# Optimization experiments

Measured on AMD Instinct MI355X. Metric: run time of the kernel, lower is better.

The kernel has to match this reference:

```python
import jax, jax.numpy as jnp
import numpy as np

B, T, D, H, L = 4, 2048, 256, 4, 2
HD = D // H
VOCAB, MAX_BITS, MLP_H = 32, 64, 64


def setup_inputs() -> dict:
    key = jax.random.key(0)
    ks = jax.random.split(key, 20)
    s = 0.02
    n = lambda k, shp: (jax.random.normal(k, shp, jnp.float32) * s)
    inp = {
        'tokens': jax.random.randint(ks[0], (B, T), 0, VOCAB),
        'embed': n(ks[1], (VOCAB, D)),
        'ln1_w': jnp.ones((L, D)), 'ln1_b': jnp.zeros((L, D)),
        'qkv_w': n(ks[2], (L, D, 3 * D)), 'qkv_b': jnp.zeros((L, 3 * D)),
        'proj_w': n(ks[3], (L, D, D)), 'proj_b': jnp.zeros((L, D)),
        'ln2_w': jnp.ones((L, D)), 'ln2_b': jnp.zeros((L, D)),
        'ffn1_w': n(ks[4], (L, D, 4 * D)), 'ffn1_b': jnp.zeros((L, 4 * D)),
        'ffn2_w': n(ks[5], (L, 4 * D, D)), 'ffn2_b': jnp.zeros((L, D)),
        'lnf_w': jnp.ones((D,)), 'lnf_b': jnp.zeros((D,)),
        'out_queries': n(ks[6], (MAX_BITS * 2, D)),
        'outp_w': n(ks[7], (D, 1)), 'outp_b': jnp.zeros((1,)),
        'mlp_w1': n(ks[8], (3, MLP_H)), 'mlp_b1': jnp.zeros((MLP_H,)),
        'mlp_w2': n(ks[9], (MLP_H, MLP_H)), 'mlp_b2': jnp.zeros((MLP_H,)),
        'mlp_w3': n(ks[10], (MLP_H, 2)), 'mlp_b3': jnp.zeros((2,)),
    }
    return inp


def _layernorm(x, w, b, eps=1e-5):
    mu = jnp.mean(x, axis=-1, keepdims=True)
    var = jnp.mean(jnp.square(x - mu), axis=-1, keepdims=True)
    return (x - mu) * jax.lax.rsqrt(var + eps) * w + b


def _rope_tables(t_len, hd):
    inv_freq = 1.0 / (10000.0 ** (jnp.arange(0, hd, 2, dtype=jnp.float32) / hd))
    freqs = jnp.outer(jnp.arange(t_len, dtype=jnp.float32), inv_freq)  # [T, hd/2]
    emb = jnp.concatenate([freqs, freqs], axis=-1)                     # [T, hd]
    return jnp.cos(emb)[None, :, None, :], jnp.sin(emb)[None, :, None, :]


def _rotate_half(x):
    x1, x2 = x[..., : x.shape[-1] // 2], x[..., x.shape[-1] // 2:]
    return jnp.concatenate([-x2, x1], axis=-1)


def _attention(x, qkv_w, qkv_b, proj_w, proj_b):
    b, t, c = x.shape
    qkv = (x @ qkv_w + qkv_b).reshape(b, t, 3, H, HD)
    q, k, v = qkv[:, :, 0], qkv[:, :, 1], qkv[:, :, 2]  # [B,T,H,HD]
    cos, sin = _rope_tables(t, HD)
    q = q * cos + _rotate_half(q) * sin
    k = k * cos + _rotate_half(k) * sin
    scores = jnp.einsum('bthd,bshd->bhts', q, k) / jnp.sqrt(jnp.float32(HD))
    causal = jnp.tril(jnp.ones((t, t), dtype=bool))
    scores = jnp.where(causal, scores, -jnp.inf)
    attn = jax.nn.softmax(scores, axis=-1)
    out = jnp.einsum('bhts,bshd->bthd', attn, v).reshape(b, t, c)
    return out @ proj_w + proj_b


def reference(tokens, embed, ln1_w, ln1_b, qkv_w, qkv_b, proj_w, proj_b,
              ln2_w, ln2_b, ffn1_w, ffn1_b, ffn2_w, ffn2_b, lnf_w, lnf_b,
              out_queries, outp_w, outp_b,
              mlp_w1, mlp_b1, mlp_w2, mlp_b2, mlp_w3, mlp_b3):
    x = embed[tokens]  # [B,T,D]
    for l in range(L):
        x = x + _attention(_layernorm(x, ln1_w[l], ln1_b[l]),
                           qkv_w[l], qkv_b[l], proj_w[l], proj_b[l])
        h = _layernorm(x, ln2_w[l], ln2_b[l])
        h = jax.nn.gelu(h @ ffn1_w[l] + ffn1_b[l], approximate=False)
        x = x + (h @ ffn2_w[l] + ffn2_b[l])
    x = _layernorm(x, lnf_w, lnf_b)
    # query cross-attention for bit-pair selection
    q_scores = jnp.einsum('qd,btd->bqt', out_queries, x) / jnp.sqrt(jnp.float32(D))
    q_attn = jax.nn.softmax(q_scores, axis=-1)           # [B, 2*MAX_BITS, T]
    selected = jnp.einsum('bqt,btd->bqd', q_attn, x)
    bits = jax.nn.sigmoid((selected @ outp_w + outp_b)[..., 0])
    pairs = bits.reshape(-1, MAX_BITS, 2)                # [B, MAX_BITS, 2]

    # sequential full-adder over bits
    def step(carry, ab):  # carry [B], ab [B,2]
        z = jnp.concatenate([ab, carry[:, None]], axis=-1)  # [B,3]
        h = jax.nn.relu(z @ mlp_w1 + mlp_b1)
        h = jax.nn.relu(h @ mlp_w2 + mlp_b2)
        o = jax.nn.sigmoid(h @ mlp_w3 + mlp_b3)
        return o[:, 1], o[:, 0]

    carry0 = jnp.zeros((pairs.shape[0],), jnp.float32)
    carry, sum_bits = jax.lax.scan(step, carry0, jnp.swapaxes(pairs, 0, 1))
    sum_all = jnp.concatenate([sum_bits.T, carry[:, None]], axis=1)  # [B, MAX_BITS+1]
    return sum_all, pairs, q_attn
```

## Files before the change

### kernel.cpp

```cpp
#include <hip/hip_runtime.h>
#include <hip/hip_bf16.h>

#define BB 4
#define TT 2048
#define DD 256
#define HH 4
#define HDD 64
#define NROW 8192
#define NQ 128

typedef __hip_bfloat16 bf16;
typedef __attribute__((ext_vector_type(8))) short bf8v;
typedef __attribute__((ext_vector_type(4))) short bf4v;
typedef __attribute__((ext_vector_type(4))) float f4v;
typedef __attribute__((ext_vector_type(2))) unsigned int u2v;

__device__ __forceinline__ bf16 f2b(float v){ return __float2bfloat16(v); }
__device__ __forceinline__ short f2bs(float v){
    bf16 h = __float2bfloat16(v);
    return *reinterpret_cast<short*>(&h);
}
__device__ __forceinline__ float bs2f(short s){
    bf16 h = *reinterpret_cast<bf16*>(&s);
    return __bfloat162float(h);
}
__device__ __forceinline__ float rl(float v, int l){
    return __uint_as_float(__builtin_amdgcn_readlane(__float_as_uint(v), l));
}

#define DPP_ROR_ADD(v, ctrl) \
    ((v) + __int_as_float(__builtin_amdgcn_update_dpp(0, __float_as_int(v), (ctrl), 0xF, 0xF, false)))
#define DPP_ROR_MAX(v, ctrl) \
    fmaxf((v), __int_as_float(__builtin_amdgcn_update_dpp(0, __float_as_int(v), (ctrl), 0xF, 0xF, false)))

__device__ __forceinline__ void plswap16(float v, float& a, float& b){
#if __has_builtin(__builtin_amdgcn_permlane16_swap)
    u2v r = __builtin_amdgcn_permlane16_swap(__float_as_uint(v), __float_as_uint(v), false, false);
    a = __uint_as_float(r.x); b = __uint_as_float(r.y);
#else
    a = v; b = v;
    asm volatile("" : "+v"(b));
    asm("v_permlane16_swap_b32 %0, %1" : "+v"(a), "+v"(b));
#endif
}
__device__ __forceinline__ void plswap32(float v, float& a, float& b){
#if __has_builtin(__builtin_amdgcn_permlane32_swap)
    u2v r = __builtin_amdgcn_permlane32_swap(__float_as_uint(v), __float_as_uint(v), false, false);
    a = __uint_as_float(r.x); b = __uint_as_float(r.y);
#else
    a = v; b = v;
    asm volatile("" : "+v"(b));
    asm("v_permlane32_swap_b32 %0, %1" : "+v"(a), "+v"(b));
#endif
}
__device__ __forceinline__ float swap16_add(float v){ float a,b; plswap16(v,a,b); return a + b; }
__device__ __forceinline__ float swap32_add(float v){ float a,b; plswap32(v,a,b); return a + b; }
__device__ __forceinline__ float swap16_max(float v){ float a,b; plswap16(v,a,b); return fmaxf(a,b); }
__device__ __forceinline__ float swap32_max(float v){ float a,b; plswap32(v,a,b); return fmaxf(a,b); }
__device__ __forceinline__ float wsum(float v){
    v = DPP_ROR_ADD(v, 0x121); v = DPP_ROR_ADD(v, 0x122);
    v = DPP_ROR_ADD(v, 0x124); v = DPP_ROR_ADD(v, 0x128);
    v = swap16_add(v); v = swap32_add(v);
    return v;
}
__device__ __forceinline__ float wmax(float v){
    v = DPP_ROR_MAX(v, 0x121); v = DPP_ROR_MAX(v, 0x122);
    v = DPP_ROR_MAX(v, 0x124); v = DPP_ROR_MAX(v, 0x128);
    v = swap16_max(v); v = swap32_max(v);
    return v;
}

#define MFMA32(A,B,C) __builtin_amdgcn_mfma_f32_16x16x32_bf16((A),(B),(C),0,0,0)
#if __has_builtin(__builtin_amdgcn_mfma_f32_16x16x16bf16_1k)
#define MFMA16(A,B,C) __builtin_amdgcn_mfma_f32_16x16x16bf16_1k((A),(B),(C),0,0,0)
#else
__device__ __forceinline__ f4v mfma16_asm(bf4v a, bf4v b, f4v c){
    f4v d;
    asm("v_mfma_f32_16x16x16_bf16 %0, %1, %2, %3" : "=v"(d) : "v"(a), "v"(b), "v"(c));
    return d;
}
#define MFMA16(A,B,C) mfma16_asm((A),(B),(C))
#endif

__global__ __launch_bounds__(256) void k_embln(const int* __restrict__ tok,
                                               const float* __restrict__ emb,
                                               const float* __restrict__ w,
                                               const float* __restrict__ b,
                                               float* __restrict__ x,
                                               bf16* __restrict__ Y){
    int row = blockIdx.x*4 + (threadIdx.x >> 6);
    int lane = threadIdx.x & 63;
    f4v v = *(const f4v*)(emb + (long)tok[row]*DD + lane*4);
    *(f4v*)(x + (long)row*DD + lane*4) = v;
    float s  = (v[0]+v[1]) + (v[2]+v[3]);
    float s2 = (v[0]*v[0]+v[1]*v[1]) + (v[2]*v[2]+v[3]*v[3]);
    s = wsum(s); s2 = wsum(s2);
    float mu  = s * (1.0f/DD);
    float var = s2 * (1.0f/DD) - mu*mu;
    float rs  = rsqrtf(var + 1e-5f);
    f4v wv4 = *(const f4v*)(w + lane*4);
    f4v bv4 = *(const f4v*)(b + lane*4);
    bf4v o;
    #pragma unroll
    for (int i=0;i<4;i++) o[i] = f2bs((v[i]-mu)*rs*wv4[i] + bv4[i]);
    *(bf4v*)(Y + (long)row*DD + lane*4) = o;
}

__global__ __launch_bounds__(256) void k_wtall(const float* __restrict__ qkvw,
                                               const float* __restrict__ projw,
                                               const float* __restrict__ f1w,
                                               const float* __restrict__ f2w,
                                               bf16* __restrict__ wt,
                                               const float* __restrict__ oq, bf16* __restrict__ oqb,
                                               float* __restrict__ cosT, float* __restrict__ sinT,
                                               const float* __restrict__ w2, float* __restrict__ w2t){
    __shared__ float t[32][33];
    int z = blockIdx.z;
    if (z == 8){
        int bid = blockIdx.y*32 + blockIdx.x;
        if (bid >= 256) return;
        int gid = bid*256 + threadIdx.y*32 + threadIdx.x;
        int tt = gid >> 5, dd = gid & 31;
        float invf = powf(10000.0f, -(float)(2*dd)/64.0f);
        float ang = (float)tt * invf;
        float sn, cs;
        sincosf(ang, &sn, &cs);
        cosT[gid] = cs; sinT[gid] = sn;
        if (gid < NQ*DD) oqb[gid] = f2b(oq[gid]);
        if (gid < 4096){ int j = gid >> 6, k = gid & 63; w2t[gid] = w2[k*64 + j]; }
        return;
    }
    int l = z >> 2, type = z & 3;
    long L = (long)l*786432;
    int K, M; const float* src; long doff;
    if (type == 0){ K=256;  M=768;  src = qkvw + (long)l*256*768;  doff = L; }
    else if (type == 1){ K=256;  M=256;  src = projw + (long)l*256*256; doff = L + 196608; }
    else if (type == 2){ K=256;  M=1024; src = f1w  + (long)l*256*1024; doff = L + 262144; }
    else               { K=1024; M=256;  src = f2w  + (long)l*1024*256; doff = L + 524288; }
    int m0 = blockIdx.x*32, k0 = blockIdx.y*32;
    if (m0 >= M || k0 >= K) return;
    bf16* dst = wt + doff;
    int tx = threadIdx.x, ty = threadIdx.y;
    #pragma unroll
    for (int i=0;i<4;i++)
        t[ty+i*8][tx] = src[(long)(k0+ty+i*8)*M + m0 + tx];
    __syncthreads();
    #pragma unroll
    for (int i=0;i<4;i++)
        dst[(long)(m0+ty+i*8)*K + k0 + tx] = f2b(t[tx][ty+i*8]);
}

__global__ __launch_bounds__(256) void k_lnb(const float* __restrict__ X,
                                             const float* __restrict__ w,
                                             const float* __restrict__ b,
                                             bf16* __restrict__ Y){
    int row = blockIdx.x*4 + (threadIdx.x >> 6);
    int lane = threadIdx.x & 63;
    f4v v = *(const f4v*)(X + (long)row*DD + lane*4);
    float s  = (v[0]+v[1]) + (v[2]+v[3]);
    float s2 = (v[0]*v[0]+v[1]*v[1]) + (v[2]*v[2]+v[3]*v[3]);
    s = wsum(s); s2 = wsum(s2);
    float mu  = s * (1.0f/DD);
    float var = s2 * (1.0f/DD) - mu*mu;
    float rs  = rsqrtf(var + 1e-5f);
    f4v wv4 = *(const f4v*)(w + lane*4);
    f4v bv4 = *(const f4v*)(b + lane*4);
    bf4v o;
    #pragma unroll
    for (int i=0;i<4;i++) o[i] = f2bs((v[i]-mu)*rs*wv4[i] + bv4[i]);
    *(bf4v*)(Y + (long)row*DD + lane*4) = o;
}

__global__ __launch_bounds__(256) void k_lnf(const float* __restrict__ X,
                                             const float* __restrict__ w,
                                             const float* __restrict__ b,
                                             const float* __restrict__ ow,
                                             bf16* __restrict__ Yb,
                                             float* __restrict__ g){
    int row = blockIdx.x*4 + (threadIdx.x >> 6);
    int lane = threadIdx.x & 63;
    f4v v = *(const f4v*)(X + (long)row*DD + lane*4);
    float s  = (v[0]+v[1]) + (v[2]+v[3]);
    float s2 = (v[0]*v[0]+v[1]*v[1]) + (v[2]*v[2]+v[3]*v[3]);
    s = wsum(s); s2 = wsum(s2);
    float mu  = s * (1.0f/DD);
    float var = s2 * (1.0f/DD) - mu*mu;
    float rs  = rsqrtf(var + 1e-5f);
    f4v wv4 = *(const f4v*)(w + lane*4);
    f4v bv4 = *(const f4v*)(b + lane*4);
    f4v ov4 = *(const f4v*)(ow + lane*4);
    bf4v o;
    float gp = 0.f;
    #pragma unroll
    for (int i=0;i<4;i++){
        float y = (v[i]-mu)*rs*wv4[i] + bv4[i];
        o[i] = f2bs(y);
        gp += y * ov4[i];
    }
    *(bf4v*)(Yb + (long)row*DD + lane*4) = o;
    gp = wsum(gp);
    if (lane == 0) g[row] = gp;
}

__global__ __launch_bounds__(256) void k_mgemm(const bf16* __restrict__ A,
                                               const bf16* __restrict__ Wt,
                                               const float* __restrict__ bias,
                                               float* __restrict__ Cf,
                                               bf16* __restrict__ Cb,
                                               int K, int M, int mode){
    __shared__ short As[2][128*64];
    __shared__ short Ws[2][64*64];
    int tid = threadIdx.x;
    int lane = tid & 63, wv = tid >> 6;
    int n0 = blockIdx.y * 128, m0 = blockIdx.x * 64;
    int rbase = (wv >> 1) * 64, cbase = (wv & 1) * 32;
    f4v acc[4][2] = {};
    bf8v va[4], vw[2];
    #pragma unroll
    for (int c=0;c<4;c++){
        int idx = c*256 + tid;
        va[c] = *(const bf8v*)(A + (long)(n0 + (idx>>3))*K + ((idx&7)<<3));
    }
    #pragma unroll
    for (int c=0;c<2;c++){
        int idx = c*256 + tid;
        vw[c] = *(const bf8v*)(Wt + (long)(m0 + (idx>>3))*K + ((idx&7)<<3));
    }
    int buf = 0;
    for (int k0 = 0; k0 < K; k0 += 64){
        #pragma unroll
        for (int c=0;c<4;c++){
            int idx = c*256 + tid, row = idx>>3;
            *(bf8v*)&As[buf][row*64 + (((idx&7)<<3) ^ ((row&7)<<3))] = va[c];
        }
        #pragma unroll
        for (int c=0;c<2;c++){
            int idx = c*256 + tid, row = idx>>3;
            *(bf8v*)&Ws[buf][row*64 + (((idx&7)<<3) ^ ((row&7)<<3))] = vw[c];
        }
        __syncthreads();
        if (k0 + 64 < K){
            #pragma unroll
            for (int c=0;c<4;c++){
                int idx = c*256 + tid;
                va[c] = *(const bf8v*)(A + (long)(n0 + (idx>>3))*K + k0 + 64 + ((idx&7)<<3));
            }
            #pragma unroll
            for (int c=0;c<2;c++){
                int idx = c*256 + tid;
                vw[c] = *(const bf8v*)(Wt + (long)(m0 + (idx>>3))*K + k0 + 64 + ((idx&7)<<3));
            }
        }
        int k8 = (lane >> 4) << 3;
        #pragma unroll
        for (int h=0; h<2; h++){
            bf8v af[4], bfr[2];
            #pragma unroll
            for (int i=0;i<4;i++){
                int row = rbase + i*16 + (lane&15);
                af[i] = *(bf8v*)&As[buf][row*64 + ((h*32 + k8) ^ ((row&7)<<3))];
            }
            #pragma unroll
            for (int j=0;j<2;j++){
                int row = cbase + j*16 + (lane&15);
                bfr[j] = *(bf8v*)&Ws[buf][row*64 + ((h*32 + k8) ^ ((row&7)<<3))];
            }
            #pragma unroll
            for (int i=0;i<4;i++)
                #pragma unroll
                for (int j=0;j<2;j++)
                    acc[i][j] = MFMA32(af[i], bfr[j], acc[i][j]);
        }
        buf ^= 1;
    }
    int rq = (lane >> 4) * 4;
    int cl = lane & 15;
    #pragma unroll
    for (int i=0;i<4;i++){
        #pragma unroll
        for (int j=0;j<2;j++){
            int m = m0 + cbase + j*16 + cl;
            float bs = bias[m];
            #pragma unroll
            for (int r=0;r<4;r++){
                int n = n0 + rbase + i*16 + rq + r;
                float v = acc[i][j][r] + bs;
                long idx = (long)n*M + m;
                if (mode == 0)      Cf[idx] = v;
                else if (mode == 1) Cf[idx] += v;
                else if (mode == 2) Cb[idx] = f2b(0.5f*v*(1.0f + erff(v*0.70710678118654752f)));
                else                Cb[idx] = f2b(v);
            }
        }
    }
}

__global__ __launch_bounds__(256) void k_mgemmQKV(const bf16* __restrict__ A,
                                                  const bf16* __restrict__ Wt,
                                                  const float* __restrict__ bias,
                                                  const float* __restrict__ cosT,
                                                  const float* __restrict__ sinT,
                                                  bf16* __restrict__ qb,
                                                  bf16* __restrict__ kb,
                                                  bf16* __restrict__ vt){
    __shared__ short As[128*64];
    __shared__ short Ws[64*64];
    __shared__ short E[128][68];
    const int K = 256, M = 768;
    int tid = threadIdx.x;
    int lane = tid & 63, wv = tid >> 6;
    int n0 = blockIdx.y * 128, m0 = blockIdx.x * 64;
    int rbase = (wv >> 1) * 64, cbase = (wv & 1) * 32;
    f4v acc[4][2] = {};
    for (int k0 = 0; k0 < K; k0 += 64){
        bf8v va[4], vw[2];
        #pragma unroll
        for (int c=0;c<4;c++){
            int idx = c*256 + tid;
            va[c] = *(const bf8v*)(A + (long)(n0 + (idx>>3))*K + k0 + ((idx&7)<<3));
        }
        #pragma unroll
        for (int c=0;c<2;c++){
            int idx = c*256 + tid;
            vw[c] = *(const bf8v*)(Wt + (long)(m0 + (idx>>3))*K + k0 + ((idx&7)<<3));
        }
        __syncthreads();
        #pragma unroll
        for (int c=0;c<4;c++){
            int idx = c*256 + tid, row = idx>>3;
            *(bf8v*)&As[row*64 + (((idx&7)<<3) ^ ((row&7)<<3))] = va[c];
        }
        #pragma unroll
        for (int c=0;c<2;c++){
            int idx = c*256 + tid, row = idx>>3;
            *(bf8v*)&Ws[row*64 + (((idx&7)<<3) ^ ((row&7)<<3))] = vw[c];
        }
        __syncthreads();
        int k8 = (lane >> 4) << 3;
        #pragma unroll
        for (int h=0; h<2; h++){
            bf8v af[4], bfr[2];
            #pragma unroll
            for (int i=0;i<4;i++){
                int row = rbase + i*16 + (lane&15);
                af[i] = *(bf8v*)&As[row*64 + ((h*32 + k8) ^ ((row&7)<<3))];
            }
            #pragma unroll
            for (int j=0;j<2;j++){
                int row = cbase + j*16 + (lane&15);
                bfr[j] = *(bf8v*)&Ws[row*64 + ((h*32 + k8) ^ ((row&7)<<3))];
            }
            #pragma unroll
            for (int i=0;i<4;i++)
                #pragma unroll
                for (int j=0;j<2;j++)
                    acc[i][j] = MFMA32(af[i], bfr[j], acc[i][j]);
        }
    }
    int rq = (lane >> 4) * 4;
    int cl = lane & 15;
    #pragma unroll
    for (int i=0;i<4;i++){
        #pragma unroll
        for (int j=0;j<2;j++){
            int cc = cbase + j*16 + cl;
            float bs = bias[m0 + cc];
            #pragma unroll
            for (int r=0;r<4;r++)
                E[rbase + i*16 + rq + r][cc] = f2bs(acc[i][j][r] + bs);
        }
    }
    __syncthreads();
    int part = m0 >> 8;
    int h = (m0 >> 6) & 3;
    int b = n0 >> 11;
    int t0 = n0 & 2047;
    int bh = b*HH + h;
    if (part < 2){
        bf16* dst0 = part ? kb : qb;
        int r2 = tid >> 2;
        int c0 = (tid & 3) * 16;
        int cpx = c0 ^ 32;
        #pragma unroll
        for (int half=0; half<2; half++){
            int row = half*64 + r2;
            int t = t0 + row;
            bf8v e0 = *(bf8v*)&E[row][c0];
            bf8v e1 = *(bf8v*)&E[row][c0+8];
            bf8v p0 = *(bf8v*)&E[row][cpx];
            bf8v p1 = *(bf8v*)&E[row][cpx+8];
            const float* ct = cosT + t*32;
            const float* st = sinT + t*32;
            short o[16];
            #pragma unroll
            for (int i=0;i<8;i++){
                int d = c0 + i, dd = d & 31;
                float cs = ct[dd], sn = st[dd];
                float v = bs2f(e0[i]), v2 = bs2f(p0[i]);
                o[i] = f2bs((d < 32) ? (v*cs - v2*sn) : (v*cs + v2*sn));
            }
            #pragma unroll
            for (int i=0;i<8;i++){
                int d = c0 + 8 + i, dd = d & 31;
                float cs = ct[dd], sn = st[dd];
                float v = bs2f(e1[i]), v2 = bs2f(p1[i]);
                o[8+i] = f2bs((d < 32) ? (v*cs - v2*sn) : (v*cs + v2*sn));
            }
            short* dp = (short*)dst0 + ((long)bh*TT + t)*64 + c0;
            *(bf8v*)dp     = *(bf8v*)&o[0];
            *(bf8v*)(dp+8) = *(bf8v*)&o[8];
        }
    } else {
        int tIdx0 = t0 >> 6;
        int d  = (tid & 127) >> 1;
        int k0 = (tid & 1) * 32;
        int tt = tid >> 7;
        short o[32];
        #pragma unroll
        for (int k=0;k<32;k++) o[k] = E[tt*64 + k0 + k][d];
        short* dp = (short*)vt + (((long)bh*32 + tIdx0 + tt)*64 + d)*64 + k0;
        *(bf8v*)dp      = *(bf8v*)&o[0];
        *(bf8v*)(dp+8)  = *(bf8v*)&o[8];
        *(bf8v*)(dp+16) = *(bf8v*)&o[16];
        *(bf8v*)(dp+24) = *(bf8v*)&o[24];
    }
}

__global__ __launch_bounds__(256) void k_fattn(const bf16* __restrict__ qb,
                                               const bf16* __restrict__ kb,
                                               const bf16* __restrict__ vt,
                                               bf16* __restrict__ ob){
    __shared__ short Ks[2][64][72];
    __shared__ short Vs[2][64][68];
    int bh = blockIdx.y;
    int qt = (int)(gridDim.x - 1) - (int)blockIdx.x;
    int tid = threadIdx.x;
    int lane = tid & 63, w = tid >> 6;
    int col = lane & 15, quad = lane >> 4;
    int q0 = qt*64 + w*16;
    const bf16* qp = qb + ((long)bh*TT + q0 + col)*64 + quad*8;
    bf8v bq0 = *(const bf8v*)(qp);
    bf8v bq1 = *(const bf8v*)(qp + 32);
    f4v oc[4] = {};
    float lsum = 0.f;
    int qglob = q0 + col;
    int srow = tid >> 2, sc0 = (tid & 3) * 16;
    const short* kgb = (const short*)kb + ((long)bh*TT + srow)*64 + sc0;
    const short* vgb = (const short*)vt + (((long)bh*32)*64 + srow)*64 + sc0;

    bf8v pk0 = *(const bf8v*)kgb;
    bf8v pk1 = *(const bf8v*)(kgb + 8);
    bf8v pv0 = *(const bf8v*)vgb;
    bf8v pv1 = *(const bf8v*)(vgb + 8);
    *(bf8v*)&Ks[0][srow][sc0]     = pk0;
    *(bf8v*)&Ks[0][srow][sc0 + 8] = pk1;
    *(bf8v*)&Vs[0][srow][sc0]     = pv0;
    *(bf8v*)&Vs[0][srow][sc0 + 8] = pv1;

    int buf = 0;
    for (int kt=0; kt<=qt; kt++){
        __syncthreads();
        bool more = (kt < qt);
        if (more){
            const short* kg = kgb + (long)(kt+1)*4096;
            const short* vg = vgb + (long)(kt+1)*4096;
            pk0 = *(const bf8v*)kg;
            pk1 = *(const bf8v*)(kg + 8);
            pv0 = *(const bf8v*)vg;
            pv1 = *(const bf8v*)(vg + 8);
        }
        bool diag = (kt == qt);
        int ntmax = diag ? w : 3;
        bf4v bp[4];
        #pragma unroll
        for (int nt=0; nt<4; nt++){
            if (nt > ntmax) continue;
            bf8v ka0 = *(const bf8v*)&Ks[buf][nt*16 + col][quad*8];
            bf8v ka1 = *(const bf8v*)&Ks[buf][nt*16 + col][32 + quad*8];
            f4v st = {};
            st = MFMA32(ka0, bq0, st);
            st = MFMA32(ka1, bq1, st);
            int key0 = kt*64 + nt*16 + quad*4;
            bf4v pb;
            #pragma unroll
            for (int r=0; r<4; r++){
                float e = __expf(st[r]*0.125f);
                if (diag && (key0 + r > qglob)) e = 0.f;
                lsum += e;
                pb[r] = f2bs(e);
            }
            bp[nt] = pb;
        }
        #pragma unroll
        for (int dt=0; dt<4; dt++){
            #pragma unroll
            for (int nt=0; nt<4; nt++){
                if (nt > ntmax) continue;
                bf4v va = *(const bf4v*)&Vs[buf][dt*16 + col][nt*16 + quad*4];
                oc[dt] = MFMA16(va, bp[nt], oc[dt]);
            }
        }
        if (more){
            *(bf8v*)&Ks[buf^1][srow][sc0]     = pk0;
            *(bf8v*)&Ks[buf^1][srow][sc0 + 8] = pk1;
            *(bf8v*)&Vs[buf^1][srow][sc0]     = pv0;
            *(bf8v*)&Vs[buf^1][srow][sc0 + 8] = pv1;
        }
        buf ^= 1;
    }
    lsum += __shfl_xor(lsum, 16, 64);
    lsum += __shfl_xor(lsum, 32, 64);
    float linv = 1.0f / lsum;

    int b = bh / HH, h = bh % HH;
    long obase = ((long)b*TT + q0 + col)*DD + h*64 + quad*4;
    #pragma unroll
    for (int dt=0; dt<4; dt++){
        bf4v o4;
        #pragma unroll
        for (int r=0; r<4; r++) o4[r] = f2bs(oc[dt][r]*linv);
        *(bf4v*)(ob + obase + dt*16) = o4;
    }
}

__global__ __launch_bounds__(256) void k_score(const bf16* __restrict__ oqb,
                                               const bf16* __restrict__ xfb,
                                               float* __restrict__ S){
    int b = blockIdx.y, t0 = blockIdx.x*64;
    int tid = threadIdx.x, lane = tid & 63, w = tid >> 6;
    int col = lane & 15, quad = lane >> 4, k8 = quad << 3;
    const bf16* xb = xfb + (long)b*TT*DD;
    f4v acc[2][4] = {};
    #pragma unroll
    for (int ko=0; ko<8; ko++){
        int kk = ko*32 + k8;
        bf8v a0 = *(const bf8v*)(oqb + (long)(w*32 +      col)*DD + kk);
        bf8v a1 = *(const bf8v*)(oqb + (long)(w*32 + 16 + col)*DD + kk);
        #pragma unroll
        for (int bt=0; bt<4; bt++){
            bf8v bv = *(const bf8v*)(xb + (long)(t0 + bt*16 + col)*DD + kk);
            acc[0][bt] = MFMA32(a0, bv, acc[0][bt]);
            acc[1][bt] = MFMA32(a1, bv, acc[1][bt]);
        }
    }
    #pragma unroll
    for (int qt2=0; qt2<2; qt2++){
        #pragma unroll
        for (int bt=0; bt<4; bt++){
            #pragma unroll
            for (int r=0; r<4; r++){
                int q = w*32 + qt2*16 + quad*4 + r;
                S[((long)b*NQ + q)*TT + t0 + bt*16 + col] = acc[qt2][bt][r]*0.0625f;
            }
        }
    }
}

__global__ __launch_bounds__(256) void k_psoft(const float* __restrict__ S,
                                               const float* __restrict__ g,
                                               const float* __restrict__ obias,
                                               float* __restrict__ out_qattn,
                                               float* __restrict__ out_pairs,
                                               float* __restrict__ bits){
    __shared__ float cmax[4], cs[4], cg[4];
    int bq = blockIdx.x, b = bq >> 7;
    int tid = threadIdx.x, wv = tid >> 6, lane = tid & 63;
    const f4v* S4 = (const f4v*)(S + (long)bq*TT);
    f4v s0 = S4[tid], s1 = S4[tid + 256];
    float lmax = fmaxf(fmaxf(fmaxf(s0[0],s0[1]), fmaxf(s0[2],s0[3])),
                       fmaxf(fmaxf(s1[0],s1[1]), fmaxf(s1[2],s1[3])));
    lmax = wmax(lmax);
    if (lane == 0) cmax[wv] = lmax;
    __syncthreads();
    float m = fmaxf(fmaxf(cmax[0],cmax[1]), fmaxf(cmax[2],cmax[3]));
    const f4v* g4 = (const f4v*)(g + (long)b*TT);
    f4v gv0 = g4[tid], gv1 = g4[tid + 256];
    f4v e0, e1;
    #pragma unroll
    for (int i=0;i<4;i++){ e0[i] = __expf(s0[i]-m); e1[i] = __expf(s1[i]-m); }
    float lsum = (e0[0]+e0[1]+e0[2]+e0[3]) + (e1[0]+e1[1]+e1[2]+e1[3]);
    float gdot = (e0[0]*gv0[0]+e0[1]*gv0[1]+e0[2]*gv0[2]+e0[3]*gv0[3])
               + (e1[0]*gv1[0]+e1[1]*gv1[1]+e1[2]*gv1[2]+e1[3]*gv1[3]);
    lsum = wsum(lsum); gdot = wsum(gdot);
    if (lane == 0){ cs[wv] = lsum; cg[wv] = gdot; }
    __syncthreads();
    float Lr = (cs[0]+cs[1]) + (cs[2]+cs[3]);
    float G  = (cg[0]+cg[1]) + (cg[2]+cg[3]);
    float inv = 1.0f / Lr;
    f4v* out4 = (f4v*)(out_qattn + (long)bq*TT);
    out4[tid]       = e0 * inv;
    out4[tid + 256] = e1 * inv;
    if (tid == 0){
        float bit = 1.0f/(1.0f + expf(-(G*inv + obias[0])));
        bits[bq] = bit;
        out_pairs[bq] = bit;
    }
}

__global__ __launch_bounds__(64) void k_scan(const float* __restrict__ bits,
                                             const float* __restrict__ w1, const float* __restrict__ b1,
                                             const float* __restrict__ w2t, const float* __restrict__ b2,
                                             const float* __restrict__ w3, const float* __restrict__ b3,
                                             float* __restrict__ out_sum){
    __shared__ __align__(16) float h1s[2][64];
    int b = blockIdx.x, lane = threadIdx.x;
    float w1c0 = w1[lane], w1c1 = w1[64 + lane], w1c2 = w1[128 + lane];
    float b1v = b1[lane], b2v = b2[lane];
    float w3c0 = w3[lane*2 + 0], w3c1 = w3[lane*2 + 1];
    float b30 = b3[0], b31 = b3[1];
    const f4v* wrow = (const f4v*)(w2t + (long)lane*64);
    f4v c0v = wrow[0],  c1v = wrow[1],  c2v = wrow[2],  c3v = wrow[3],
        c4v = wrow[4],  c5v = wrow[5],  c6v = wrow[6],  c7v = wrow[7],
        c8v = wrow[8],  c9v = wrow[9],  cav = wrow[10], cbv = wrow[11],
        ccv = wrow[12], cdv = wrow[13], cev = wrow[14], cfv = wrow[15];
    float z0v = bits[b*128 + lane*2 + 0];
    float z1v = bits[b*128 + lane*2 + 1];
    float carry = 0.f;
    float a1 = rl(z0v, 0)*w1c0 + rl(z1v, 0)*w1c1 + b1v;
    for (int step=0; step<64; step++){
        float h1 = fmaxf(carry*w1c2 + a1, 0.f);
        float* hb = h1s[step & 1];
        hb[lane] = h1;
        __syncthreads();
        if (step < 63){
            a1 = rl(z0v, step+1)*w1c0 + rl(z1v, step+1)*w1c1 + b1v;
        }
        const f4v* hv = (const f4v*)hb;
        f4v va = hv[0]*c0v,  vb = hv[1]*c1v,  vc = hv[2]*c2v,   vd = hv[3]*c3v;
        va += hv[4]*c4v;   vb += hv[5]*c5v;   vc += hv[6]*c6v;   vd += hv[7]*c7v;
        va += hv[8]*c8v;   vb += hv[9]*c9v;   vc += hv[10]*cav;  vd += hv[11]*cbv;
        va += hv[12]*ccv;  vb += hv[13]*cdv;  vc += hv[14]*cev;  vd += hv[15]*cfv;
        f4v vs = (va + vb) + (vc + vd);
        float h2 = fmaxf(((vs[0] + vs[1]) + (vs[2] + vs[3])) + b2v, 0.f);
        float t0 = h2*w3c0, t1 = h2*w3c1;
        t0 = DPP_ROR_ADD(t0, 0x121); t1 = DPP_ROR_ADD(t1, 0x121);
        t0 = DPP_ROR_ADD(t0, 0x122); t1 = DPP_ROR_ADD(t1, 0x122);
        t0 = DPP_ROR_ADD(t0, 0x124); t1 = DPP_ROR_ADD(t1, 0x124);
        t0 = DPP_ROR_ADD(t0, 0x128); t1 = DPP_ROR_ADD(t1, 0x128);
        t0 = swap16_add(t0); t1 = swap16_add(t1);
        t0 = swap32_add(t0); t1 = swap32_add(t1);
        float o0 = 1.0f/(1.0f + __expf(-(t0 + b30)));
        carry    = 1.0f/(1.0f + __expf(-(t1 + b31)));
        if (lane == 0) out_sum[b*65 + step] = o0;
    }
    if (lane == 0) out_sum[b*65 + 64] = carry;
}

extern "C" void kernel_launch(void* const* d_in, const int* in_sizes, int n_in,
                              void* d_out, int out_size, void* d_ws, size_t ws_size,
                              hipStream_t stream){
    const int*   tok   = (const int*)d_in[0];
    const float* emb   = (const float*)d_in[1];
    const float* ln1w  = (const float*)d_in[2];
    const float* ln1b  = (const float*)d_in[3];
    const float* qkvw  = (const float*)d_in[4];
    const float* qkvb  = (const float*)d_in[5];
    const float* projw = (const float*)d_in[6];
    const float* projb = (const float*)d_in[7];
    const float* ln2w  = (const float*)d_in[8];
    const float* ln2b  = (const float*)d_in[9];
    const float* f1w   = (const float*)d_in[10];
    const float* f1b   = (const float*)d_in[11];
    const float* f2w   = (const float*)d_in[12];
    const float* f2bb  = (const float*)d_in[13];
    const float* lnfw  = (const float*)d_in[14];
    const float* lnfb  = (const float*)d_in[15];
    const float* oq    = (const float*)d_in[16];
    const float* ow    = (const float*)d_in[17];
    const float* obias = (const float*)d_in[18];
    const float* w1    = (const float*)d_in[19];
    const float* b1    = (const float*)d_in[20];
    const float* w2    = (const float*)d_in[21];
    const float* b2    = (const float*)d_in[22];
    const float* w3    = (const float*)d_in[23];
    const float* b3    = (const float*)d_in[24];
    float* out = (float*)d_out;

    const long MB = 1048576;
    char* W = (char*)d_ws;
    float* x     = (float*)(W);
    bf16*  attnb = (bf16*)(W + 8*MB);
    bf16*  hb    = (bf16*)(W + 16*MB);
    bf16*  qb    = (bf16*)(W + 32*MB);
    bf16*  kb    = (bf16*)(W + 36*MB);
    bf16*  vt    = (bf16*)(W + 44*MB);
    bf16*  xnb   = (bf16*)(W + 48*MB);
    bf16*  wt    = (bf16*)(W + 52*MB);
    float* bits  = (float*)(W + 55*MB);
    bf16*  oqb   = (bf16*)(W + 56*MB);
    float* cosT  = (float*)(W + 57*MB);
    float* sinT  = cosT + 65536;
    float* w2t   = (float*)(W + 58*MB);
    bf16*  xfb   = (bf16*)(W + 32*MB);
    float* g     = (float*)(W + 36*MB);
    float* S     = (float*)(W + 40*MB);

    k_wtall<<<dim3(32, 32, 9), dim3(32,8), 0, stream>>>(qkvw, projw, f1w, f2w, wt,
                                                        oq, oqb, cosT, sinT, w2, w2t);

    k_embln<<<NROW/4, 256, 0, stream>>>(tok, emb, ln1w, ln1b, x, xnb);
    for (int l=0; l<2; l++){
        long L = (long)l*786432;
        if (l) k_lnb<<<NROW/4, 256, 0, stream>>>(x, ln1w + l*DD, ln1b + l*DD, xnb);
        k_mgemmQKV<<<dim3(768/64, 64), 256, 0, stream>>>(
            xnb, wt + L, qkvb + l*768, cosT, sinT, qb, kb, vt);
        k_fattn<<<dim3(TT/64, BB*HH), 256, 0, stream>>>(qb, kb, vt, attnb);
        k_mgemm<<<dim3(256/64, 64), 256, 0, stream>>>(
            attnb, wt + L + 196608, projb + l*DD, x, (bf16*)0, 256, 256, 1);
        k_lnb<<<NROW/4, 256, 0, stream>>>(x, ln2w + l*DD, ln2b + l*DD, xnb);
        k_mgemm<<<dim3(1024/64, 64), 256, 0, stream>>>(
            xnb, wt + L + 262144, f1b + l*1024, (float*)0, hb, 256, 1024, 2);
        k_mgemm<<<dim3(256/64, 64), 256, 0, stream>>>(
            hb, wt + L + 524288, f2bb + l*DD, x, (bf16*)0, 1024, 256, 1);
    }
    k_lnf<<<NROW/4, 256, 0, stream>>>(x, lnfw, lnfb, ow, xfb, g);
    k_score<<<dim3(TT/64, BB), 256, 0, stream>>>(oqb, xfb, S);
    k_psoft<<<BB*NQ, 256, 0, stream>>>(S, g, obias, out + 772, out + 260, bits);
    k_scan<<<4, 64, 0, stream>>>(bits, w1, b1, w2t, b2, w3, b3, out);
}
```

Baseline: 377.5 us.

## Add 64x64-tile double-buffered GEMM for N=256 outputs and prioritize MFMA in attention

Adds a new GEMM kernel with 64-row tiles, register-prefetched double-buffered LDS and an XOR-swizzled shared layout, and uses it for the projection and FFN2 GEMMs. With M=256 these previously launched only 256 blocks of 128 rows, and the smaller tiles launch 512 blocks to fill more of the GPU's compute units. Separately, the flash-attention kernel raises wave priority around its MFMA sections with s_setprio to improve interleaving of matrix and exp work between waves. Smaller tiles reduce data reuse per block, and the priority hints may have no effect.

```diff
diff --git a/kernel.cpp b/kernel.cpp
--- a/kernel.cpp
+++ b/kernel.cpp
@@ -295,6 +295,87 @@
     }
 }
 
+__global__ __launch_bounds__(256) void k_mgemm64(const bf16* __restrict__ A,
+                                                 const bf16* __restrict__ Wt,
+                                                 const float* __restrict__ bias,
+                                                 float* __restrict__ Cf,
+                                                 bf16* __restrict__ Cb,
+                                                 int K, int M, int mode){
+    __shared__ short As[2][64*64];
+    __shared__ short Ws[2][64*64];
+    int tid = threadIdx.x;
+    int lane = tid & 63, wv = tid >> 6;
+    int n0 = blockIdx.y * 64, m0 = blockIdx.x * 64;
+    int rbase = (wv >> 1) * 32, cbase = (wv & 1) * 32;
+    f4v acc[2][2] = {};
+    bf8v va[2], vw[2];
+    #pragma unroll
+    for (int c=0;c<2;c++){
+        int idx = c*256 + tid;
+        va[c] = *(const bf8v*)(A  + (long)(n0 + (idx>>3))*K + ((idx&7)<<3));
+        vw[c] = *(const bf8v*)(Wt + (long)(m0 + (idx>>3))*K + ((idx&7)<<3));
+    }
+    int buf = 0;
+    for (int k0 = 0; k0 < K; k0 += 64){
+        #pragma unroll
+        for (int c=0;c<2;c++){
+            int idx = c*256 + tid, row = idx>>3;
+            *(bf8v*)&As[buf][row*64 + (((idx&7)<<3) ^ ((row&7)<<3))] = va[c];
+            *(bf8v*)&Ws[buf][row*64 + (((idx&7)<<3) ^ ((row&7)<<3))] = vw[c];
+        }
+        __syncthreads();
+        if (k0 + 64 < K){
+            #pragma unroll
+            for (int c=0;c<2;c++){
+                int idx = c*256 + tid;
+                va[c] = *(const bf8v*)(A  + (long)(n0 + (idx>>3))*K + k0 + 64 + ((idx&7)<<3));
+                vw[c] = *(const bf8v*)(Wt + (long)(m0 + (idx>>3))*K + k0 + 64 + ((idx&7)<<3));
+            }
+        }
+        int k8 = (lane >> 4) << 3;
+        #pragma unroll
+        for (int h=0; h<2; h++){
+            bf8v af[2], bfr[2];
+            #pragma unroll
+            for (int i=0;i<2;i++){
+                int row = rbase + i*16 + (lane&15);
+                af[i] = *(bf8v*)&As[buf][row*64 + ((h*32 + k8) ^ ((row&7)<<3))];
+            }
+            #pragma unroll
+            for (int j=0;j<2;j++){
+                int row = cbase + j*16 + (lane&15);
+                bfr[j] = *(bf8v*)&Ws[buf][row*64 + ((h*32 + k8) ^ ((row&7)<<3))];
+            }
+            #pragma unroll
+            for (int i=0;i<2;i++)
+                #pragma unroll
+                for (int j=0;j<2;j++)
+                    acc[i][j] = MFMA32(af[i], bfr[j], acc[i][j]);
+        }
+        buf ^= 1;
+    }
+    int rq = (lane >> 4) * 4;
+    int cl = lane & 15;
+    #pragma unroll
+    for (int i=0;i<2;i++){
+        #pragma unroll
+        for (int j=0;j<2;j++){
+            int m = m0 + cbase + j*16 + cl;
+            float bs = bias[m];
+            #pragma unroll
+            for (int r=0;r<4;r++){
+                int n = n0 + rbase + i*16 + rq + r;
+                float v = acc[i][j][r] + bs;
+                long idx = (long)n*M + m;
+                if (mode == 0)      Cf[idx] = v;
+                else if (mode == 1) Cf[idx] += v;
+                else if (mode == 2) Cb[idx] = f2b(0.5f*v*(1.0f + erff(v*0.70710678118654752f)));
+                else                Cb[idx] = f2b(v);
+            }
+        }
+    }
+}
+
 __global__ __launch_bounds__(256) void k_mgemmQKV(const bf16* __restrict__ A,
                                                   const bf16* __restrict__ Wt,
                                                   const float* __restrict__ bias,
@@ -477,9 +558,11 @@
             if (nt > ntmax) continue;
             bf8v ka0 = *(const bf8v*)&Ks[buf][nt*16 + col][quad*8];
             bf8v ka1 = *(const bf8v*)&Ks[buf][nt*16 + col][32 + quad*8];
+            __builtin_amdgcn_s_setprio(1);
             f4v st = {};
             st = MFMA32(ka0, bq0, st);
             st = MFMA32(ka1, bq1, st);
+            __builtin_amdgcn_s_setprio(0);
             int key0 = kt*64 + nt*16 + quad*4;
             bf4v pb;
             #pragma unroll
@@ -491,6 +574,7 @@
             }
             bp[nt] = pb;
         }
+        __builtin_amdgcn_s_setprio(1);
         #pragma unroll
         for (int dt=0; dt<4; dt++){
             #pragma unroll
@@ -500,6 +584,7 @@
                 oc[dt] = MFMA16(va, bp[nt], oc[dt]);
             }
         }
+        __builtin_amdgcn_s_setprio(0);
         if (more){
             *(bf8v*)&Ks[buf^1][srow][sc0]     = pk0;
             *(bf8v*)&Ks[buf^1][srow][sc0 + 8] = pk1;
@@ -705,12 +790,12 @@
         k_mgemmQKV<<<dim3(768/64, 64), 256, 0, stream>>>(
             xnb, wt + L, qkvb + l*768, cosT, sinT, qb, kb, vt);
         k_fattn<<<dim3(TT/64, BB*HH), 256, 0, stream>>>(qb, kb, vt, attnb);
-        k_mgemm<<<dim3(256/64, 64), 256, 0, stream>>>(
+        k_mgemm64<<<dim3(256/64, NROW/64), 256, 0, stream>>>(
             attnb, wt + L + 196608, projb + l*DD, x, (bf16*)0, 256, 256, 1);
         k_lnb<<<NROW/4, 256, 0, stream>>>(x, ln2w + l*DD, ln2b + l*DD, xnb);
         k_mgemm<<<dim3(1024/64, 64), 256, 0, stream>>>(
             xnb, wt + L + 262144, f1b + l*1024, (float*)0, hb, 256, 1024, 2);
-        k_mgemm<<<dim3(256/64, 64), 256, 0, stream>>>(
+        k_mgemm64<<<dim3(256/64, NROW/64), 256, 0, stream>>>(
             hb, wt + L + 524288, f2bb + l*DD, x, (bf16*)0, 1024, 256, 1);
     }
     k_lnf<<<NROW/4, 256, 0, stream>>>(x, lnfw, lnfb, ow, xfb, g);
```

After: 365.5 us. 1.03x faster.
